# Kernel tuning notes

Hardware: AMD Instinct MI355X
Metric: run time of the kernel (lower is better)

The kernel has to match this reference:

```python
import jax, jax.numpy as jnp
import numpy as np

N_NODES = 50000


def _sage_conv(x, src, dst, W_l, b_l, W_r, n_nodes):
    # mean-aggregate neighbor (source) features onto targets
    msg = x[src]                                   # [E, d_in] gather
    agg = jax.ops.segment_sum(msg, dst, num_segments=n_nodes)   # [N, d_in]
    deg = jax.ops.segment_sum(jnp.ones((src.shape[0],), x.dtype), dst,
                              num_segments=n_nodes)
    agg = agg / jnp.clip(deg, 1.0, None)[:, None]  # mean with deg>=1 clamp (PyG)
    # out = lin_l(agg) + lin_r(x)   (bias lives in lin_l)
    return agg @ W_l.T + b_l + x @ W_r.T


def setup_inputs() -> dict:
    key = jax.random.key(0)
    ks = jax.random.split(key, 8)
    d_in, d_hid, d_out = 128, 256, 128
    n_edges = 800000
    x = jax.random.normal(ks[0], (N_NODES, d_in), dtype=jnp.float32)
    edge_index = jax.random.randint(ks[1], (2, n_edges), 0, N_NODES, dtype=jnp.int32)
    def glorot(k, shape):
        lim = float(np.sqrt(6.0 / (shape[0] + shape[1])))
        return jax.random.uniform(k, shape, jnp.float32, -lim, lim)
    return {
        "x": x,
        "edge_index": edge_index,
        "W1l": glorot(ks[2], (d_hid, d_in)),
        "b1": jnp.zeros((d_hid,), jnp.float32),
        "W1r": glorot(ks[3], (d_hid, d_in)),
        "W2l": glorot(ks[4], (d_out, d_hid)),
        "b2": jnp.zeros((d_out,), jnp.float32),
        "W2r": glorot(ks[5], (d_out, d_hid)),
    }


def reference(x, edge_index, W1l, b1, W1r, W2l, b2, W2r):
    src, dst = edge_index[0], edge_index[1]
    h = jax.nn.relu(_sage_conv(x, src, dst, W1l, b1, W1r, N_NODES))
    out = _sage_conv(h, src, dst, W2l, b2, W2r, N_NODES)
    return out
```

## Files before the change

### kernel.cpp

```cpp
#include <hip/hip_runtime.h>
#include <hip/hip_bf16.h>

#define NN 50000
#define NN_PAD 50176
#define NE 800000
#define NB 196
#define CAP 6144
#define EPB 4096

typedef __attribute__((ext_vector_type(8))) short short8;
typedef __attribute__((ext_vector_type(4))) float f32x4;
typedef __attribute__((ext_vector_type(2))) float f32x2;
typedef __attribute__((ext_vector_type(4))) unsigned int u32x4;
typedef __attribute__((ext_vector_type(2))) unsigned int u32x2;

__device__ __forceinline__ unsigned short f2bf(float f) {
    union { float f; unsigned u; } v; v.f = f;
    unsigned u = v.u;
    return (unsigned short)((u + 0x7fffu + ((u >> 16) & 1u)) >> 16);
}
__device__ __forceinline__ float bfu_lo(unsigned u) {
    union { unsigned u; float f; } v; v.u = u << 16; return v.f;
}
__device__ __forceinline__ float bfu_hi(unsigned u) {
    union { unsigned u; float f; } v; v.u = u & 0xffff0000u; return v.f;
}
__device__ __forceinline__ void acc_fp8(float* acc, uint2 q) {
    f32x2 a0 = __builtin_amdgcn_cvt_pk_f32_fp8(q.x, false);
    f32x2 a1 = __builtin_amdgcn_cvt_pk_f32_fp8(q.x, true);
    f32x2 a2 = __builtin_amdgcn_cvt_pk_f32_fp8(q.y, false);
    f32x2 a3 = __builtin_amdgcn_cvt_pk_f32_fp8(q.y, true);
    acc[0] += a0.x; acc[1] += a0.y; acc[2] += a1.x; acc[3] += a1.y;
    acc[4] += a2.x; acc[5] += a2.y; acc[6] += a3.x; acc[7] += a3.y;
}


__global__ void k_setup_part(const float* __restrict__ W1l, const float* __restrict__ W1r,
                             const float* __restrict__ W2l, const float* __restrict__ W2r,
                             unsigned short* __restrict__ W1pk, unsigned short* __restrict__ W2pk,
                             const float* __restrict__ x, unsigned short* __restrict__ Apk,
                             unsigned char* __restrict__ x_f8,
                             const int* __restrict__ src, const int* __restrict__ dst,
                             int* __restrict__ gcursor, unsigned* __restrict__ pairs) {
    int blk = blockIdx.x, t = threadIdx.x;
    if (blk < NB) {
        __shared__ int cnt[256];
        __shared__ int cur[256];
        __shared__ int base[256];
        cnt[t] = 0; cur[t] = 0;
        __syncthreads();
        int e0 = blk * EPB;
        int eend = min(e0 + EPB, NE);
        for (int e = e0 + t; e < eend; e += 256)
            atomicAdd(&cnt[dst[e] >> 8], 1);
        __syncthreads();
        if (t < NB && cnt[t] > 0) base[t] = t * CAP + atomicAdd(&gcursor[t], cnt[t]);
        __syncthreads();
        for (int e = e0 + t; e < eend; e += 256) {
            int s = src[e], d = dst[e];
            int bk = d >> 8;
            int pos = base[bk] + atomicAdd(&cur[bk], 1);
            if (pos < (bk + 1) * CAP) pairs[pos] = ((unsigned)s << 8) | (unsigned)(d & 255);
        }
    } else if (blk < 260) {
        int tid = (blk - 196) * 256 + t;
        int table = tid >> 13;
        int r = tid & 8191;
        int lane = r & 63, ni = (r >> 6) & 3, ks = (r >> 8) & 7, g = r >> 11;
        int lm = lane & 15, lq = lane >> 4;
        int o = g * 64 + ni * 16 + lm;
        int k = ks * 32 + lq * 8;
        unsigned short v[8];
        if (table == 0) {
            if (k < 128) {
#pragma unroll
                for (int j = 0; j < 8; ++j) v[j] = f2bf(W1l[o * 128 + k + j]);
            } else {
#pragma unroll
                for (int j = 0; j < 8; ++j) v[j] = f2bf(W1r[o * 128 + k - 128 + j]);
            }
            *(uint4*)(W1pk + (size_t)r * 8) = *(const uint4*)v;
        } else {
            if (o < 128) {
#pragma unroll
                for (int j = 0; j < 8; ++j) v[j] = f2bf(W2l[o * 256 + k + j]);
            } else {
#pragma unroll
                for (int j = 0; j < 8; ++j) v[j] = f2bf(W2r[(o - 128) * 256 + k + j]);
            }
            *(uint4*)(W2pk + (size_t)r * 8) = *(const uint4*)v;
        }
    } else {
        int gid = (blk - 260) * 256 + t;
        int n = gid >> 5, c = gid & 31;
        f32x4 v = __builtin_nontemporal_load((const f32x4*)x + (size_t)n * 32 + c);
        unsigned short o[4];
        o[0] = f2bf(v[0]); o[1] = f2bf(v[1]); o[2] = f2bf(v[2]); o[3] = f2bf(v[3]);
        int k = 128 + c * 4;
        int ks = k >> 5, lq = (k >> 3) & 3, j0 = k & 7;
        int tile = n >> 6, r = n & 63, mi = r >> 4, lm = r & 15;
        *(u32x2*)(Apk + (size_t)tile * 16384 +
                  ((size_t)((ks * 4 + mi) * 64 + lm + 16 * lq)) * 8 + j0) = *(const u32x2*)o;
        unsigned p = (unsigned)__builtin_amdgcn_cvt_pk_fp8_f32(v[0], v[1], 0, false);
        p = (unsigned)__builtin_amdgcn_cvt_pk_fp8_f32(v[2], v[3], (int)p, true);
        *(unsigned*)(x_f8 + (size_t)n * 128 + c * 4) = p;
    }
}

__global__ void k_build(const int* __restrict__ gcursor, const unsigned* __restrict__ pairs,
                        unsigned* __restrict__ meta, unsigned short* __restrict__ esrc) {
    __shared__ int buf[256];
    __shared__ int ldeg[256];
    __shared__ int cur[256];
    __shared__ int sh_base, sh_cnt;
    __shared__ unsigned short lsrc[CAP];
    __shared__ unsigned lp[CAP];
    int b = blockIdx.x, t = threadIdx.x;
    int c = (t < NB) ? min(gcursor[t], CAP) : 0;
    if (t < 256) buf[t] = c;
    __syncthreads();
#pragma unroll
    for (int o = 1; o < 256; o <<= 1) {
        int add = (t < 256 && t >= o) ? buf[t - o] : 0;
        __syncthreads();
        if (t < 256) buf[t] += add;
        __syncthreads();
    }
    if (t == b) { sh_cnt = c; sh_base = buf[b] - c; }
    if (t < 256) ldeg[t] = 0;
    __syncthreads();
    int cnt = sh_cnt, base = sh_base;
    for (int e = t; e < cnt; e += 1024) {
        unsigned p = pairs[(size_t)b * CAP + e];
        lp[e] = p;
        atomicAdd(&ldeg[p & 255u], 1);
    }
    __syncthreads();
    int v = (t < 256) ? ldeg[t] : 0;
    if (t < 256) buf[t] = v;
    __syncthreads();
#pragma unroll
    for (int o = 1; o < 256; o <<= 1) {
        int add = (t < 256 && t >= o) ? buf[t - o] : 0;
        __syncthreads();
        if (t < 256) buf[t] += add;
        __syncthreads();
    }
    if (t < 256) {
        int lst = buf[t] - v;
        cur[t] = lst;
        int node = b * 256 + t;
        meta[node] = (node < NN) ? ((unsigned)(base + lst) | ((unsigned)v << 20)) : 0u;
    }
    __syncthreads();
    for (int e = t; e < cnt; e += 1024) {
        unsigned p = lp[e];
        int pos = atomicAdd(&cur[p & 255u], 1);
        lsrc[pos] = (unsigned short)(p >> 8);
    }
    __syncthreads();
    for (int e = t; e < cnt; e += 1024) esrc[base + e] = lsrc[e];
}

__global__ void k_agg1(const uint2* __restrict__ xf8, const unsigned* __restrict__ meta,
                       const unsigned short* __restrict__ esrc,
                       unsigned short* __restrict__ Apk) {
    int gid = blockIdx.x * blockDim.x + threadIdx.x;
    int n = gid >> 4, c = gid & 15;
    unsigned mt = meta[n];
    int st = (int)(mt & 0xFFFFFu), dg = (int)(mt >> 20);
    float acc[8] = {0.f, 0.f, 0.f, 0.f, 0.f, 0.f, 0.f, 0.f};
    int i = 0;
    for (; i + 8 <= dg; i += 8) {
        int s0 = esrc[st + i],     s1 = esrc[st + i + 1];
        int s2 = esrc[st + i + 2], s3 = esrc[st + i + 3];
        int s4 = esrc[st + i + 4], s5 = esrc[st + i + 5];
        int s6 = esrc[st + i + 6], s7 = esrc[st + i + 7];
        uint2 q0 = xf8[(size_t)s0 * 16 + c];
        uint2 q1 = xf8[(size_t)s1 * 16 + c];
        uint2 q2 = xf8[(size_t)s2 * 16 + c];
        uint2 q3 = xf8[(size_t)s3 * 16 + c];
        uint2 q4 = xf8[(size_t)s4 * 16 + c];
        uint2 q5 = xf8[(size_t)s5 * 16 + c];
        uint2 q6 = xf8[(size_t)s6 * 16 + c];
        uint2 q7 = xf8[(size_t)s7 * 16 + c];
        acc_fp8(acc, q0); acc_fp8(acc, q1); acc_fp8(acc, q2); acc_fp8(acc, q3);
        acc_fp8(acc, q4); acc_fp8(acc, q5); acc_fp8(acc, q6); acc_fp8(acc, q7);
    }
    for (; i < dg; ++i) {
        int s = esrc[st + i];
        acc_fp8(acc, xf8[(size_t)s * 16 + c]);
    }
    float invd = 1.0f / (float)max(dg, 1);
    unsigned short o[8];
#pragma unroll
    for (int j = 0; j < 8; ++j) o[j] = f2bf(acc[j] * invd);
    int ks = c >> 2, lq = c & 3;
    int tile = n >> 6, r = n & 63, mi = r >> 4, lm = r & 15;
    *(u32x4*)(Apk + (size_t)tile * 16384 +
              ((size_t)((ks * 4 + mi) * 64 + lm + 16 * lq)) * 8) = *(const u32x4*)o;
}

__global__ __launch_bounds__(256, 2) void k_gemm12(
        const unsigned short* __restrict__ Apk,
        const unsigned short* __restrict__ W1pk, const unsigned short* __restrict__ W2pk,
        const float* __restrict__ b1, const float* __restrict__ b2,
        unsigned char* __restrict__ y2f8, unsigned short* __restrict__ Sbf) {
    __shared__ unsigned short T[16384];
    int t = threadIdx.x, blk = blockIdx.x;
    int wave = t >> 6, lane = t & 63;
    int lm = lane & 15, lq = lane >> 4;
    int pbase = lm * 4 + lq;

    short8 w[8][4];
    {
        const unsigned short* wb = W1pk + (size_t)wave * 16384;
#pragma unroll
        for (int ks = 0; ks < 8; ++ks)
#pragma unroll
            for (int ni = 0; ni < 4; ++ni)
                w[ks][ni] = *(const short8*)(wb + ((size_t)((ks * 4 + ni) * 64 + lane)) * 8);
    }

    const unsigned short* apk = Apk + (size_t)blk * 16384;
    f32x4 acc1[4][4];
#pragma unroll
    for (int mi = 0; mi < 4; ++mi)
#pragma unroll
        for (int ni = 0; ni < 4; ++ni) acc1[mi][ni] = (f32x4){0.f, 0.f, 0.f, 0.f};
#pragma unroll
    for (int ks = 0; ks < 8; ++ks) {
        short8 a[4];
#pragma unroll
        for (int mi = 0; mi < 4; ++mi)
            a[mi] = *(const short8*)(apk + ((size_t)((ks * 4 + mi) * 64 + lane)) * 8);
#pragma unroll
        for (int mi = 0; mi < 4; ++mi)
#pragma unroll
            for (int ni = 0; ni < 4; ++ni)
                acc1[mi][ni] = __builtin_amdgcn_mfma_f32_16x16x32_bf16(a[mi], w[ks][ni], acc1[mi][ni], 0, 0, 0);
    }

    {
        const unsigned short* wb = W2pk + (size_t)wave * 16384;
#pragma unroll
        for (int ks = 0; ks < 8; ++ks)
#pragma unroll
            for (int ni = 0; ni < 4; ++ni)
                w[ks][ni] = *(const short8*)(wb + ((size_t)((ks * 4 + ni) * 64 + lane)) * 8);
    }

#pragma unroll
    for (int ni = 0; ni < 4; ++ni) {
        int col = wave * 64 + ni * 16 + lm;
        float bv = b1[col];
        int ks = col >> 5;
        int la = (col & 31) >> 3, j = col & 7;
#pragma unroll
        for (int mi = 0; mi < 4; ++mi)
#pragma unroll
            for (int r = 0; r < 4; ++r) {
                float v = fmaxf(acc1[mi][ni][r] + bv, 0.0f);
                T[((size_t)((ks * 4 + mi) * 64 + (lq * 4 + r) * 4 + la)) * 8 + j] = f2bf(v);
            }
    }
    __syncthreads();

    f32x4 acc2[4][4];
#pragma unroll
    for (int mi = 0; mi < 4; ++mi)
#pragma unroll
        for (int ni = 0; ni < 4; ++ni) acc2[mi][ni] = (f32x4){0.f, 0.f, 0.f, 0.f};
#pragma unroll
    for (int ks = 0; ks < 8; ++ks) {
        short8 a[4];
#pragma unroll
        for (int mi = 0; mi < 4; ++mi)
            a[mi] = *(const short8*)(T + ((size_t)((ks * 4 + mi) * 64 + pbase)) * 8);
#pragma unroll
        for (int mi = 0; mi < 4; ++mi)
#pragma unroll
            for (int ni = 0; ni < 4; ++ni)
                acc2[mi][ni] = __builtin_amdgcn_mfma_f32_16x16x32_bf16(a[mi], w[ks][ni], acc2[mi][ni], 0, 0, 0);
    }
    __syncthreads();

    {
        unsigned char* T8 = (unsigned char*)T;
        unsigned short* T16 = (unsigned short*)T + 4096;
        if (wave < 2) {
#pragma unroll
            for (int ni = 0; ni < 4; ++ni) {
                int col = wave * 64 + ni * 16 + lm;
#pragma unroll
                for (int mi = 0; mi < 4; ++mi)
#pragma unroll
                    for (int r = 0; r < 4; ++r) {
                        int rl = mi * 16 + lq * 4 + r;
                        float v = acc2[mi][ni][r];
                        unsigned p = (unsigned)__builtin_amdgcn_cvt_pk_fp8_f32(v, v, 0, false);
                        T8[rl * 128 + col] = (unsigned char)(p & 0xff);
                    }
            }
        } else {
#pragma unroll
            for (int ni = 0; ni < 4; ++ni) {
                int col = (wave - 2) * 64 + ni * 16 + lm;
                float bv = b2[col];
#pragma unroll
                for (int mi = 0; mi < 4; ++mi)
#pragma unroll
                    for (int r = 0; r < 4; ++r) {
                        int rl = mi * 16 + lq * 4 + r;
                        T16[rl * 128 + col] = f2bf(acc2[mi][ni][r] + bv);
                    }
            }
        }
    }
    __syncthreads();

    {
        const uint4* Ty = (const uint4*)T;
        uint4* gy = (uint4*)(y2f8 + (size_t)blk * 64 * 128);
        gy[t] = Ty[t];
        gy[t + 256] = Ty[t + 256];
        const u32x4* Ts = (const u32x4*)((const char*)T + 8192);
        u32x4* gs = (u32x4*)(Sbf + (size_t)blk * 64 * 128);
#pragma unroll
        for (int i = 0; i < 4; ++i)
            __builtin_nontemporal_store(Ts[t + i * 256], &gs[t + i * 256]);
    }
}

__global__ void k_agg_out(const uint2* __restrict__ yf8, const unsigned short* __restrict__ Sbf,
                          const unsigned* __restrict__ meta,
                          const unsigned short* __restrict__ esrc,
                          float* __restrict__ out) {
    int gid = blockIdx.x * blockDim.x + threadIdx.x;
    int n = gid >> 4, c = gid & 15;
    unsigned mt = meta[n];
    int st = (int)(mt & 0xFFFFFu), dg = (int)(mt >> 20);
    float acc[8] = {0.f, 0.f, 0.f, 0.f, 0.f, 0.f, 0.f, 0.f};
    int i = 0;
    for (; i + 8 <= dg; i += 8) {
        int s0 = esrc[st + i],     s1 = esrc[st + i + 1];
        int s2 = esrc[st + i + 2], s3 = esrc[st + i + 3];
        int s4 = esrc[st + i + 4], s5 = esrc[st + i + 5];
        int s6 = esrc[st + i + 6], s7 = esrc[st + i + 7];
        uint2 q0 = yf8[(size_t)s0 * 16 + c];
        uint2 q1 = yf8[(size_t)s1 * 16 + c];
        uint2 q2 = yf8[(size_t)s2 * 16 + c];
        uint2 q3 = yf8[(size_t)s3 * 16 + c];
        uint2 q4 = yf8[(size_t)s4 * 16 + c];
        uint2 q5 = yf8[(size_t)s5 * 16 + c];
        uint2 q6 = yf8[(size_t)s6 * 16 + c];
        uint2 q7 = yf8[(size_t)s7 * 16 + c];
        acc_fp8(acc, q0); acc_fp8(acc, q1); acc_fp8(acc, q2); acc_fp8(acc, q3);
        acc_fp8(acc, q4); acc_fp8(acc, q5); acc_fp8(acc, q6); acc_fp8(acc, q7);
    }
    for (; i < dg; ++i) {
        int s = esrc[st + i];
        acc_fp8(acc, yf8[(size_t)s * 16 + c]);
    }
    float invd = 1.0f / (float)max(dg, 1);
    u32x4 sv = __builtin_nontemporal_load((const u32x4*)Sbf + (size_t)n * 16 + c);
    f32x4 o0, o1;
    o0[0] = bfu_lo(sv[0]) + acc[0] * invd; o0[1] = bfu_hi(sv[0]) + acc[1] * invd;
    o0[2] = bfu_lo(sv[1]) + acc[2] * invd; o0[3] = bfu_hi(sv[1]) + acc[3] * invd;
    o1[0] = bfu_lo(sv[2]) + acc[4] * invd; o1[1] = bfu_hi(sv[2]) + acc[5] * invd;
    o1[2] = bfu_lo(sv[3]) + acc[6] * invd; o1[3] = bfu_hi(sv[3]) + acc[7] * invd;
    f32x4* op = (f32x4*)(out + (size_t)n * 128 + c * 8);
    __builtin_nontemporal_store(o0, op);
    __builtin_nontemporal_store(o1, op + 1);
}

extern "C" void kernel_launch(void* const* d_in, const int* in_sizes, int n_in,
                              void* d_out, int out_size, void* d_ws, size_t ws_size,
                              hipStream_t stream) {
    const float* x   = (const float*)d_in[0];
    const int*   ei  = (const int*)d_in[1];
    const int*   src = ei;
    const int*   dst = ei + NE;
    const float* W1l = (const float*)d_in[2];
    const float* b1  = (const float*)d_in[3];
    const float* W1r = (const float*)d_in[4];
    const float* W2l = (const float*)d_in[5];
    const float* b2  = (const float*)d_in[6];
    const float* W2r = (const float*)d_in[7];
    float* out = (float*)d_out;

    char* ws = (char*)d_ws;
    unsigned* meta        = (unsigned*)(ws + 0);
    int* gcursor          = (int*)(ws + 401408);
    unsigned short* esrc  = (unsigned short*)(ws + 409600);
    unsigned* pairs       = (unsigned*)(ws + 4194304);
    unsigned short* Sbf   = (unsigned short*)(ws + 9437184);
    unsigned char* x_f8   = (unsigned char*)(ws + 22282240);
    unsigned char* y2f8   = (unsigned char*)(ws + 28704768);
    unsigned short* Apk   = (unsigned short*)(ws + 35651584);
    unsigned short* W1pk  = (unsigned short*)(ws + 61341696);
    unsigned short* W2pk  = (unsigned short*)(ws + 61472768);

    hipMemsetAsync(gcursor, 0, 1024, stream);
    k_setup_part<<<6510, 256, 0, stream>>>(W1l, W1r, W2l, W2r, W1pk, W2pk,
                                           x, Apk, x_f8, src, dst, gcursor, pairs);
    k_build<<<NB, 1024, 0, stream>>>(gcursor, pairs, meta, esrc);
    k_agg1<<<NN * 16 / 256, 256, 0, stream>>>((const uint2*)x_f8, meta, esrc, Apk);
    k_gemm12<<<NN_PAD / 64, 256, 0, stream>>>(Apk, W1pk, W2pk, b1, b2, y2f8, Sbf);
    k_agg_out<<<NN * 16 / 256, 256, 0, stream>>>((const uint2*)y2f8, Sbf,
                                                 meta, esrc, out);
}
```

Before: 185.8 us.

## Fuse CSR build with layer-1 aggregation using 64-node buckets

Partitioning moves from 256-node buckets (196 blocks) to 64-node buckets (784 blocks), so each bucket lines up with one GEMM tile. The CSR build and the first mean aggregation are merged into one kernel. That kernel reads source indices from shared memory and writes the packed bf16 A tile directly. This drops a kernel launch, the global esrc/meta round trip before agg1, and the global prefix scan over buckets, since each bucket now has a fixed CAP2 slot. The costs are a padded esrc layout with 21-bit offsets, and a risk of overflow if a bucket receives more than 1536 edges.

```diff
diff --git a/kernel.cpp b/kernel.cpp
--- a/kernel.cpp
+++ b/kernel.cpp
@@ -5,7 +5,8 @@
 #define NN_PAD 50176
 #define NE 800000
 #define NB 196
-#define CAP 6144
+#define NB2 784
+#define CAP2 1536
 #define EPB 4096
 
 typedef __attribute__((ext_vector_type(8))) short short8;
@@ -33,6 +34,7 @@
     acc[0] += a0.x; acc[1] += a0.y; acc[2] += a1.x; acc[3] += a1.y;
     acc[4] += a2.x; acc[5] += a2.y; acc[6] += a3.x; acc[7] += a3.y;
 }
+
 
 
 __global__ void k_setup_part(const float* __restrict__ W1l, const float* __restrict__ W1r,
@@ -44,23 +46,24 @@
                              int* __restrict__ gcursor, unsigned* __restrict__ pairs) {
     int blk = blockIdx.x, t = threadIdx.x;
     if (blk < NB) {
-        __shared__ int cnt[256];
-        __shared__ int cur[256];
-        __shared__ int base[256];
-        cnt[t] = 0; cur[t] = 0;
+        __shared__ int cnt[NB2];
+        __shared__ int cur[NB2];
+        __shared__ int base[NB2];
+        for (int k = t; k < NB2; k += 256) { cnt[k] = 0; cur[k] = 0; }
         __syncthreads();
         int e0 = blk * EPB;
         int eend = min(e0 + EPB, NE);
         for (int e = e0 + t; e < eend; e += 256)
-            atomicAdd(&cnt[dst[e] >> 8], 1);
+            atomicAdd(&cnt[dst[e] >> 6], 1);
         __syncthreads();
-        if (t < NB && cnt[t] > 0) base[t] = t * CAP + atomicAdd(&gcursor[t], cnt[t]);
+        for (int k = t; k < NB2; k += 256)
+            if (cnt[k] > 0) base[k] = k * CAP2 + atomicAdd(&gcursor[k], cnt[k]);
         __syncthreads();
         for (int e = e0 + t; e < eend; e += 256) {
             int s = src[e], d = dst[e];
-            int bk = d >> 8;
+            int bk = d >> 6;
             int pos = base[bk] + atomicAdd(&cur[bk], 1);
-            if (pos < (bk + 1) * CAP) pairs[pos] = ((unsigned)s << 8) | (unsigned)(d & 255);
+            if (pos < (bk + 1) * CAP2) pairs[pos] = ((unsigned)s << 6) | (unsigned)(d & 63);
         }
     } else if (blk < 260) {
         int tid = (blk - 196) * 256 + t;
@@ -107,98 +110,80 @@
     }
 }
 
-__global__ void k_build(const int* __restrict__ gcursor, const unsigned* __restrict__ pairs,
-                        unsigned* __restrict__ meta, unsigned short* __restrict__ esrc) {
-    __shared__ int buf[256];
-    __shared__ int ldeg[256];
-    __shared__ int cur[256];
-    __shared__ int sh_base, sh_cnt;
-    __shared__ unsigned short lsrc[CAP];
-    __shared__ unsigned lp[CAP];
+__global__ __launch_bounds__(512) void k_build_agg1(
+        const int* __restrict__ gcursor, const unsigned* __restrict__ pairs,
+        const uint2* __restrict__ xf8, unsigned short* __restrict__ esrc,
+        unsigned* __restrict__ meta, unsigned short* __restrict__ Apk) {
+    __shared__ unsigned lp[CAP2];
+    __shared__ unsigned short lsrc[CAP2];
+    __shared__ int ldeg[64];
+    __shared__ int lcur[64];
+    __shared__ int lstart[64];
     int b = blockIdx.x, t = threadIdx.x;
-    int c = (t < NB) ? min(gcursor[t], CAP) : 0;
-    if (t < 256) buf[t] = c;
-    __syncthreads();
-#pragma unroll
-    for (int o = 1; o < 256; o <<= 1) {
-        int add = (t < 256 && t >= o) ? buf[t - o] : 0;
-        __syncthreads();
-        if (t < 256) buf[t] += add;
-        __syncthreads();
-    }
-    if (t == b) { sh_cnt = c; sh_base = buf[b] - c; }
-    if (t < 256) ldeg[t] = 0;
-    __syncthreads();
-    int cnt = sh_cnt, base = sh_base;
-    for (int e = t; e < cnt; e += 1024) {
-        unsigned p = pairs[(size_t)b * CAP + e];
+    if (t < 64) ldeg[t] = 0;
+    __syncthreads();
+    int cnt = min(gcursor[b], CAP2);
+    const unsigned* pb = pairs + (size_t)b * CAP2;
+    for (int e = t; e < cnt; e += 512) {
+        unsigned p = pb[e];
         lp[e] = p;
-        atomicAdd(&ldeg[p & 255u], 1);
-    }
-    __syncthreads();
-    int v = (t < 256) ? ldeg[t] : 0;
-    if (t < 256) buf[t] = v;
-    __syncthreads();
-#pragma unroll
-    for (int o = 1; o < 256; o <<= 1) {
-        int add = (t < 256 && t >= o) ? buf[t - o] : 0;
-        __syncthreads();
-        if (t < 256) buf[t] += add;
-        __syncthreads();
-    }
-    if (t < 256) {
-        int lst = buf[t] - v;
-        cur[t] = lst;
-        int node = b * 256 + t;
-        meta[node] = (node < NN) ? ((unsigned)(base + lst) | ((unsigned)v << 20)) : 0u;
-    }
-    __syncthreads();
-    for (int e = t; e < cnt; e += 1024) {
+        atomicAdd(&ldeg[p & 63u], 1);
+    }
+    __syncthreads();
+    if (t < 64) {
+        int s = 0;
+        for (int j = 0; j < t; ++j) s += ldeg[j];
+        lstart[t] = s; lcur[t] = s;
+    }
+    __syncthreads();
+    for (int e = t; e < cnt; e += 512) {
         unsigned p = lp[e];
-        int pos = atomicAdd(&cur[p & 255u], 1);
-        lsrc[pos] = (unsigned short)(p >> 8);
-    }
-    __syncthreads();
-    for (int e = t; e < cnt; e += 1024) esrc[base + e] = lsrc[e];
-}
-
-__global__ void k_agg1(const uint2* __restrict__ xf8, const unsigned* __restrict__ meta,
-                       const unsigned short* __restrict__ esrc,
-                       unsigned short* __restrict__ Apk) {
-    int gid = blockIdx.x * blockDim.x + threadIdx.x;
-    int n = gid >> 4, c = gid & 15;
-    unsigned mt = meta[n];
-    int st = (int)(mt & 0xFFFFFu), dg = (int)(mt >> 20);
-    float acc[8] = {0.f, 0.f, 0.f, 0.f, 0.f, 0.f, 0.f, 0.f};
-    int i = 0;
-    for (; i + 8 <= dg; i += 8) {
-        int s0 = esrc[st + i],     s1 = esrc[st + i + 1];
-        int s2 = esrc[st + i + 2], s3 = esrc[st + i + 3];
-        int s4 = esrc[st + i + 4], s5 = esrc[st + i + 5];
-        int s6 = esrc[st + i + 6], s7 = esrc[st + i + 7];
-        uint2 q0 = xf8[(size_t)s0 * 16 + c];
-        uint2 q1 = xf8[(size_t)s1 * 16 + c];
-        uint2 q2 = xf8[(size_t)s2 * 16 + c];
-        uint2 q3 = xf8[(size_t)s3 * 16 + c];
-        uint2 q4 = xf8[(size_t)s4 * 16 + c];
-        uint2 q5 = xf8[(size_t)s5 * 16 + c];
-        uint2 q6 = xf8[(size_t)s6 * 16 + c];
-        uint2 q7 = xf8[(size_t)s7 * 16 + c];
-        acc_fp8(acc, q0); acc_fp8(acc, q1); acc_fp8(acc, q2); acc_fp8(acc, q3);
-        acc_fp8(acc, q4); acc_fp8(acc, q5); acc_fp8(acc, q6); acc_fp8(acc, q7);
-    }
-    for (; i < dg; ++i) {
-        int s = esrc[st + i];
-        acc_fp8(acc, xf8[(size_t)s * 16 + c]);
-    }
-    float invd = 1.0f / (float)max(dg, 1);
-    unsigned short o[8];
-#pragma unroll
-    for (int j = 0; j < 8; ++j) o[j] = f2bf(acc[j] * invd);
-    int ks = c >> 2, lq = c & 3;
-    int tile = n >> 6, r = n & 63, mi = r >> 4, lm = r & 15;
-    *(u32x4*)(Apk + (size_t)tile * 16384 +
-              ((size_t)((ks * 4 + mi) * 64 + lm + 16 * lq)) * 8) = *(const u32x4*)o;
+        int pos = atomicAdd(&lcur[p & 63u], 1);
+        lsrc[pos] = (unsigned short)(p >> 6);
+    }
+    __syncthreads();
+    for (int e = t; e < cnt; e += 512) esrc[(size_t)b * CAP2 + e] = lsrc[e];
+    if (t < 64) {
+        int node = b * 64 + t;
+        if (node < NN)
+            meta[node] = ((unsigned)(b * CAP2 + lstart[t])) | ((unsigned)ldeg[t] << 21);
+    }
+    int c = t & 15;
+#pragma unroll
+    for (int rr = 0; rr < 2; ++rr) {
+        int nl = rr * 32 + (t >> 4);
+        int st = lstart[nl], dg = ldeg[nl];
+        float acc[8] = {0.f, 0.f, 0.f, 0.f, 0.f, 0.f, 0.f, 0.f};
+        int i = 0;
+        for (; i + 8 <= dg; i += 8) {
+            int s0 = lsrc[st + i],     s1 = lsrc[st + i + 1];
+            int s2 = lsrc[st + i + 2], s3 = lsrc[st + i + 3];
+            int s4 = lsrc[st + i + 4], s5 = lsrc[st + i + 5];
+            int s6 = lsrc[st + i + 6], s7 = lsrc[st + i + 7];
+            uint2 q0 = xf8[(size_t)s0 * 16 + c];
+            uint2 q1 = xf8[(size_t)s1 * 16 + c];
+            uint2 q2 = xf8[(size_t)s2 * 16 + c];
+            uint2 q3 = xf8[(size_t)s3 * 16 + c];
+            uint2 q4 = xf8[(size_t)s4 * 16 + c];
+            uint2 q5 = xf8[(size_t)s5 * 16 + c];
+            uint2 q6 = xf8[(size_t)s6 * 16 + c];
+            uint2 q7 = xf8[(size_t)s7 * 16 + c];
+            acc_fp8(acc, q0); acc_fp8(acc, q1); acc_fp8(acc, q2); acc_fp8(acc, q3);
+            acc_fp8(acc, q4); acc_fp8(acc, q5); acc_fp8(acc, q6); acc_fp8(acc, q7);
+        }
+        for (; i < dg; ++i) {
+            int s = lsrc[st + i];
+            acc_fp8(acc, xf8[(size_t)s * 16 + c]);
+        }
+        float invd = 1.0f / (float)max(dg, 1);
+        unsigned short o[8];
+#pragma unroll
+        for (int j = 0; j < 8; ++j) o[j] = f2bf(acc[j] * invd);
+        int ks = c >> 2, lq = c & 3;
+        int mi = nl >> 4, lm = nl & 15;
+        *(u32x4*)(Apk + (size_t)b * 16384 +
+                  ((size_t)((ks * 4 + mi) * 64 + lm + 16 * lq)) * 8) = *(const u32x4*)o;
+    }
 }
 
 __global__ __launch_bounds__(256, 2) void k_gemm12(
@@ -339,7 +324,7 @@
     int gid = blockIdx.x * blockDim.x + threadIdx.x;
     int n = gid >> 4, c = gid & 15;
     unsigned mt = meta[n];
-    int st = (int)(mt & 0xFFFFFu), dg = (int)(mt >> 20);
+    int st = (int)(mt & 0x1FFFFFu), dg = (int)(mt >> 21);
     float acc[8] = {0.f, 0.f, 0.f, 0.f, 0.f, 0.f, 0.f, 0.f};
     int i = 0;
     for (; i + 8 <= dg; i += 8) {
@@ -390,23 +375,23 @@
     float* out = (float*)d_out;
 
     char* ws = (char*)d_ws;
-    unsigned* meta        = (unsigned*)(ws + 0);
-    int* gcursor          = (int*)(ws + 401408);
-    unsigned short* esrc  = (unsigned short*)(ws + 409600);
-    unsigned* pairs       = (unsigned*)(ws + 4194304);
-    unsigned short* Sbf   = (unsigned short*)(ws + 9437184);
-    unsigned char* x_f8   = (unsigned char*)(ws + 22282240);
-    unsigned char* y2f8   = (unsigned char*)(ws + 28704768);
-    unsigned short* Apk   = (unsigned short*)(ws + 35651584);
-    unsigned short* W1pk  = (unsigned short*)(ws + 61341696);
-    unsigned short* W2pk  = (unsigned short*)(ws + 61472768);
-
-    hipMemsetAsync(gcursor, 0, 1024, stream);
+    int* gcursor          = (int*)(ws + 0);
+    unsigned* meta        = (unsigned*)(ws + 4096);
+    unsigned* pairs       = (unsigned*)(ws + 204800);
+    unsigned short* esrc  = (unsigned short*)(ws + 5021696);
+    unsigned char* x_f8   = (unsigned char*)(ws + 7430144);
+    unsigned short* Sbf   = (unsigned short*)(ws + 13830144);
+    unsigned char* y2f8   = (unsigned char*)(ws + 26675200);
+    unsigned short* Apk   = (unsigned short*)(ws + 33097728);
+    unsigned short* W1pk  = (unsigned short*)(ws + 58787840);
+    unsigned short* W2pk  = (unsigned short*)(ws + 58918912);
+
+    hipMemsetAsync(gcursor, 0, 4096, stream);
     k_setup_part<<<6510, 256, 0, stream>>>(W1l, W1r, W2l, W2r, W1pk, W2pk,
                                            x, Apk, x_f8, src, dst, gcursor, pairs);
-    k_build<<<NB, 1024, 0, stream>>>(gcursor, pairs, meta, esrc);
-    k_agg1<<<NN * 16 / 256, 256, 0, stream>>>((const uint2*)x_f8, meta, esrc, Apk);
-    k_gemm12<<<NN_PAD / 64, 256, 0, stream>>>(Apk, W1pk, W2pk, b1, b2, y2f8, Sbf);
+    k_build_agg1<<<NB2, 512, 0, stream>>>(gcursor, pairs, (const uint2*)x_f8,
+                                          esrc, meta, Apk);
+    k_gemm12<<<NB2, 256, 0, stream>>>(Apk, W1pk, W2pk, b1, b2, y2f8, Sbf);
     k_agg_out<<<NN * 16 / 256, 256, 0, stream>>>((const uint2*)y2f8, Sbf,
                                                  meta, esrc, out);
 }
```

Measured after the change: 180.4 us (median of 2 runs). 2.9% less time.
